# Optimization experiments

Measured on AMD Instinct MI355X. Metric: run time of the kernel, lower is better.

Reference implementation:

```python
import jax, jax.numpy as jnp
import numpy as np

B, S, H, E, V = 64, 1024, 1024, 1024, 50257


def setup_inputs() -> dict:
    key = jax.random.key(0)
    ks = jax.random.split(key, 12)
    x = jax.random.randint(ks[0], (B, 1), 0, V, dtype=jnp.int64)
    h = jax.random.normal(ks[1], (B, H), dtype=jnp.float32)
    c = jax.random.normal(ks[2], (B, H), dtype=jnp.float32)
    encoder_output = jax.random.normal(ks[3], (B, S, H), dtype=jnp.float32)
    length = jax.random.randint(ks[4], (B,), 1, S + 1, dtype=jnp.int32)
    length = length.at[0].set(S)  # mask width is length[0]; must equal S
    scale = 0.02
    emb = jax.random.normal(ks[5], (V, E), dtype=jnp.float32) * scale
    W_ih = jax.random.normal(ks[6], (4 * H, E), dtype=jnp.float32) * scale
    b_ih = jnp.zeros((4 * H,), dtype=jnp.float32)
    W_hh = jax.random.normal(ks[7], (4 * H, H), dtype=jnp.float32) * scale
    b_hh = jnp.zeros((4 * H,), dtype=jnp.float32)
    W_bilin = jax.random.normal(ks[8], (H, H), dtype=jnp.float32) * scale
    W_out = jax.random.normal(ks[9], (V, 2 * H), dtype=jnp.float32) * scale
    b_out = jnp.zeros((V,), dtype=jnp.float32)
    return {"x": x, "h": h, "c": c, "encoder_output": encoder_output,
            "length": length, "emb": emb, "W_ih": W_ih, "b_ih": b_ih,
            "W_hh": W_hh, "b_hh": b_hh, "W_bilin": W_bilin,
            "W_out": W_out, "b_out": b_out}


def reference(x, h, c, encoder_output, length, emb, W_ih, b_ih, W_hh, b_hh,
              W_bilin, W_out, b_out):
    # embedding + squeeze(1); dropout is identity in eval mode
    xe = emb[x[:, 0]]  # [B, E]
    # LSTMCell: gates in PyTorch order i, f, g, o
    gates = xe @ W_ih.T + b_ih + h @ W_hh.T + b_hh  # [B, 4H]
    i_g, f_g, g_g, o_g = jnp.split(gates, 4, axis=-1)
    i_g = jax.nn.sigmoid(i_g)
    f_g = jax.nn.sigmoid(f_g)
    g_g = jnp.tanh(g_g)
    o_g = jax.nn.sigmoid(o_g)
    c_new = f_g * c + i_g * g_g
    h_new = o_g * jnp.tanh(c_new)  # [B, H]
    # bilinear attention energy: (h W) . enc
    energy = jnp.einsum('bh,hk,bsk->bs', h_new, W_bilin, encoder_output)
    # mask multiplies energy BEFORE softmax (faithful to original code)
    mask = (jnp.arange(S)[None, :] < length[:, None]).astype(energy.dtype)
    attn = jax.nn.softmax(energy * mask, axis=-1)  # [B, S]
    context = jnp.einsum('bs,bsh->bh', attn, encoder_output)  # [B, H]
    output = jnp.concatenate([context, h_new], axis=1) @ W_out.T + b_out  # [B, V]
    return output, h_new, c_new
```

## Files before the change

### kernel.cpp

```cpp
#include <hip/hip_runtime.h>
#include <math.h>

constexpr int NB = 64;
constexpr int NS = 1024;
constexpr int NH = 1024;
constexpr int NE = 1024;
constexpr int NV = 50257;
constexpr int NK2 = 2048;

typedef __bf16 bf16_8 __attribute__((ext_vector_type(8)));
typedef float  f32x4  __attribute__((ext_vector_type(4)));

__global__ __launch_bounds__(256) void k_cvtAg(const int* __restrict__ x,
    const float* __restrict__ h, const float* __restrict__ emb,
    __bf16* __restrict__ Ag) {
  int t = blockIdx.x * 256 + threadIdx.x;
  int b = t >> 11, k = t & 2047;
  float v = (k < NE) ? emb[(size_t)x[b] * NE + k] : h[b * NH + (k - NE)];
  Ag[t] = (__bf16)v;
}

__global__ __launch_bounds__(256) void k_gates_mfma(const __bf16* __restrict__ Ag,
    const float* __restrict__ Wih, const float* __restrict__ bih,
    const float* __restrict__ Whh, const float* __restrict__ bhh,
    float* __restrict__ gates) {
  __shared__ f32x4 red[4][4][64];
  int lane = threadIdx.x & 63;
  int wave = threadIdx.x >> 6;
  int col  = lane & 15;
  int grp  = lane >> 4;
  int j    = blockIdx.x * 16 + col;

  const float* Wsel = (wave < 2) ? Wih : Whh;
  const float*  wp  = Wsel + (size_t)j * 1024 + (wave & 1) * 512 + grp * 8;
  const __bf16* ap  = Ag + wave * 512 + grp * 8;

  f32x4 acc[4] = {};
#pragma unroll 4
  for (int ks = 0; ks < 16; ++ks) {
    int kb = ks * 32;
    float4 b0 = *(const float4*)(wp + kb);
    float4 b1 = *(const float4*)(wp + kb + 4);
    bf16_8 bf;
    bf[0] = (__bf16)b0.x; bf[1] = (__bf16)b0.y;
    bf[2] = (__bf16)b0.z; bf[3] = (__bf16)b0.w;
    bf[4] = (__bf16)b1.x; bf[5] = (__bf16)b1.y;
    bf[6] = (__bf16)b1.z; bf[7] = (__bf16)b1.w;
#pragma unroll
    for (int m = 0; m < 4; ++m) {
      bf16_8 a = *(const bf16_8*)(ap + (m * 16 + col) * NK2 + kb);
      acc[m] = __builtin_amdgcn_mfma_f32_16x16x32_bf16(a, bf, acc[m], 0, 0, 0);
    }
  }
#pragma unroll
  for (int m = 0; m < 4; ++m) red[wave][m][lane] = acc[m];
  __syncthreads();
  f32x4 s = red[0][wave][lane];
#pragma unroll
  for (int wv = 1; wv < 4; ++wv) s += red[wv][wave][lane];
  float bias = bih[j] + bhh[j];
  int b = wave * 16 + grp * 4;
#pragma unroll
  for (int r = 0; r < 4; ++r)
    gates[(b + r) * 4096 + j] = s[r] + bias;
}

__global__ __launch_bounds__(256) void k_lstm(const float* __restrict__ gates,
    const float* __restrict__ c, float* __restrict__ hc_out,
    __bf16* __restrict__ A_bf) {
  int t = blockIdx.x * 256 + threadIdx.x;
  int b = t >> 10, hh = t & 1023;
  float ig = gates[b * 4096 + hh];
  float fg = gates[b * 4096 + 1024 + hh];
  float gg = gates[b * 4096 + 2048 + hh];
  float og = gates[b * 4096 + 3072 + hh];
  float i_ = 1.f / (1.f + expf(-ig));
  float f_ = 1.f / (1.f + expf(-fg));
  float g_ = tanhf(gg);
  float o_ = 1.f / (1.f + expf(-og));
  float cn = f_ * c[t] + i_ * g_;
  float hn = o_ * tanhf(cn);
  hc_out[t] = hn;
  hc_out[NB * NH + t] = cn;
  A_bf[b * NK2 + 1024 + hh] = (__bf16)hn;
}

__global__ __launch_bounds__(256) void k_bilin(const float* __restrict__ hnew,
    const float* __restrict__ Wb, float* __restrict__ t_out) {
  int b = blockIdx.x >> 2;
  int k = ((blockIdx.x & 3) << 8) + threadIdx.x;
  const float* hb = hnew + b * NH;
  float acc = 0.f;
#pragma unroll 8
  for (int hh = 0; hh < NH; ++hh)
    acc += hb[hh] * Wb[hh * NH + k];
  t_out[b * NH + k] = acc;
}

__global__ __launch_bounds__(256) void k_attn(const float* __restrict__ t_in,
    const float* __restrict__ enc, const int* __restrict__ length,
    float* __restrict__ ctxp, float* __restrict__ ml) {
  int b     = blockIdx.x >> 4;
  int strip = ((blockIdx.x & 15) << 2) + (threadIdx.x >> 6);
  int lane  = threadIdx.x & 63;
  int len   = length[b];
  int s0    = strip * 16;

  const float4* tp4 = (const float4*)(t_in + b * NH);
  float4 tv[4];
#pragma unroll
  for (int i = 0; i < 4; ++i) tv[i] = tp4[i * 64 + lane];

  const float4* ep4 = (const float4*)(enc + ((size_t)b * NS + s0) * NH);

  float m_run = -1e30f, l_run = 0.f;
  f32x4 acc[4] = {};

#pragma unroll 2
  for (int r = 0; r < 16; ++r) {
    float4 e[4];
#pragma unroll
    for (int i = 0; i < 4; ++i) e[i] = ep4[r * 256 + i * 64 + lane];
    float d = 0.f;
#pragma unroll
    for (int i = 0; i < 4; ++i)
      d += tv[i].x * e[i].x + tv[i].y * e[i].y + tv[i].z * e[i].z + tv[i].w * e[i].w;
#pragma unroll
    for (int off = 32; off; off >>= 1) d += __shfl_xor(d, off);
    float v = (s0 + r < len) ? d : 0.f;
    float m_new = fmaxf(m_run, v);
    float f = expf(m_run - m_new);
    float w = expf(v - m_new);
    l_run = l_run * f + w;
#pragma unroll
    for (int i = 0; i < 4; ++i) {
      acc[i][0] = acc[i][0] * f + w * e[i].x;
      acc[i][1] = acc[i][1] * f + w * e[i].y;
      acc[i][2] = acc[i][2] * f + w * e[i].z;
      acc[i][3] = acc[i][3] * f + w * e[i].w;
    }
    m_run = m_new;
  }

  int idx = b * 64 + strip;
  float* P = ctxp + (size_t)idx * 1024;
#pragma unroll
  for (int i = 0; i < 4; ++i)
    *(f32x4*)(P + (i * 64 + lane) * 4) = acc[i];
  if (lane == 0) {
    ml[idx * 2]     = m_run;
    ml[idx * 2 + 1] = l_run;
  }
}

__global__ __launch_bounds__(256) void k_attn_combine(const float* __restrict__ ctxp,
    const float* __restrict__ ml, __bf16* __restrict__ A_bf) {
  int b = blockIdx.x;
  int tid = threadIdx.x;
  float M = -1e30f;
#pragma unroll
  for (int c = 0; c < 64; ++c) M = fmaxf(M, ml[(b * 64 + c) * 2]);
  float Z = 0.f;
  f32x4 num = {0.f, 0.f, 0.f, 0.f};
#pragma unroll 4
  for (int c = 0; c < 64; ++c) {
    float e = expf(ml[(b * 64 + c) * 2] - M);
    Z += e * ml[(b * 64 + c) * 2 + 1];
    f32x4 p = *(const f32x4*)(ctxp + ((size_t)(b * 64 + c)) * 1024 + tid * 4);
    num += e * p;
  }
  float inv = 1.f / Z;
  __bf16* dst = A_bf + b * NK2 + tid * 4;
#pragma unroll
  for (int i = 0; i < 4; ++i) dst[i] = (__bf16)(num[i] * inv);
}

__global__ __launch_bounds__(64) void k_out_mfma(const __bf16* __restrict__ A,
    const float* __restrict__ Wout, const float* __restrict__ bout,
    float* __restrict__ out) {
  int lane = threadIdx.x;
  int col  = lane & 15;
  int grp  = lane >> 4;
  int vb   = blockIdx.x * 32;
  int va   = vb + col;
  int vc   = vb + 16 + col;
  int vaC  = va < NV ? va : NV - 1;
  int vcC  = vc < NV ? vc : NV - 1;

  const float*  wpA = Wout + (size_t)vaC * NK2 + grp * 8;
  const float*  wpB = Wout + (size_t)vcC * NK2 + grp * 8;
  const __bf16* ap  = A + grp * 8;

  f32x4 acc[4][2] = {};

#pragma unroll 2
  for (int ks = 0; ks < 64; ++ks) {
    int kb = ks * 32;
    float4 a0 = *(const float4*)(wpA + kb);
    float4 a1 = *(const float4*)(wpA + kb + 4);
    float4 c0 = *(const float4*)(wpB + kb);
    float4 c1 = *(const float4*)(wpB + kb + 4);
    bf16_8 bfA, bfB;
    bfA[0] = (__bf16)a0.x; bfA[1] = (__bf16)a0.y;
    bfA[2] = (__bf16)a0.z; bfA[3] = (__bf16)a0.w;
    bfA[4] = (__bf16)a1.x; bfA[5] = (__bf16)a1.y;
    bfA[6] = (__bf16)a1.z; bfA[7] = (__bf16)a1.w;
    bfB[0] = (__bf16)c0.x; bfB[1] = (__bf16)c0.y;
    bfB[2] = (__bf16)c0.z; bfB[3] = (__bf16)c0.w;
    bfB[4] = (__bf16)c1.x; bfB[5] = (__bf16)c1.y;
    bfB[6] = (__bf16)c1.z; bfB[7] = (__bf16)c1.w;
#pragma unroll
    for (int m = 0; m < 4; ++m) {
      bf16_8 a = *(const bf16_8*)(ap + (size_t)(m * 16 + col) * NK2 + kb);
      acc[m][0] = __builtin_amdgcn_mfma_f32_16x16x32_bf16(a, bfA, acc[m][0], 0, 0, 0);
      acc[m][1] = __builtin_amdgcn_mfma_f32_16x16x32_bf16(a, bfB, acc[m][1], 0, 0, 0);
    }
  }

#pragma unroll
  for (int n = 0; n < 2; ++n) {
    int vrow = vb + n * 16 + col;
    if (vrow < NV) {
      float bb = bout[vrow];
      int mrow = grp * 4;
#pragma unroll
      for (int m = 0; m < 4; ++m)
#pragma unroll
        for (int r = 0; r < 4; ++r)
          out[(size_t)(m * 16 + mrow + r) * NV + vrow] = acc[m][n][r] + bb;
    }
  }
}

extern "C" void kernel_launch(void* const* d_in, const int* in_sizes, int n_in,
                              void* d_out, int out_size, void* d_ws, size_t ws_size,
                              hipStream_t stream) {
  const int*   x      = (const int*)d_in[0];
  const float* h      = (const float*)d_in[1];
  const float* c      = (const float*)d_in[2];
  const float* enc    = (const float*)d_in[3];
  const int*   length = (const int*)d_in[4];
  const float* emb    = (const float*)d_in[5];
  const float* Wih    = (const float*)d_in[6];
  const float* bih    = (const float*)d_in[7];
  const float* Whh    = (const float*)d_in[8];
  const float* bhh    = (const float*)d_in[9];
  const float* Wb     = (const float*)d_in[10];
  const float* Wout   = (const float*)d_in[11];
  const float* bout   = (const float*)d_in[12];

  float* out = (float*)d_out;
  float* hn  = out + (size_t)NB * NV;

  float* ws      = (float*)d_ws;
  float* gates   = ws;
  float* t_ws    = gates + NB * 4 * NH;
  float* ctxp    = t_ws + NB * NH;
  float* ml      = ctxp + 64 * (size_t)NB * 1024;
  __bf16* A_bf   = (__bf16*)(ml + NB * 128);
  __bf16* Ag_bf  = A_bf + NB * NK2;

  k_cvtAg<<<NB * NK2 / 256, 256, 0, stream>>>(x, h, emb, Ag_bf);
  k_gates_mfma<<<4096 / 16, 256, 0, stream>>>(Ag_bf, Wih, bih, Whh, bhh, gates);
  k_lstm<<<NB * NH / 256, 256, 0, stream>>>(gates, c, hn, A_bf);
  k_bilin<<<NB * 4, 256, 0, stream>>>(hn, Wb, t_ws);
  k_attn<<<NB * 16, 256, 0, stream>>>(t_ws, enc, length, ctxp, ml);
  k_attn_combine<<<NB, 256, 0, stream>>>(ctxp, ml, A_bf);
  k_out_mfma<<<(NV + 31) / 32, 64, 0, stream>>>(A_bf, Wout, bout, out);
}
```

Baseline: 308.1 us.

## Split attention into finer strips and restructure output GEMM with prefetch

Measured after the change: 351.2 us. 1.14x slower.

```diff
diff --git a/kernel.cpp b/kernel.cpp
--- a/kernel.cpp
+++ b/kernel.cpp
@@ -100,11 +100,11 @@
 __global__ __launch_bounds__(256) void k_attn(const float* __restrict__ t_in,
     const float* __restrict__ enc, const int* __restrict__ length,
     float* __restrict__ ctxp, float* __restrict__ ml) {
-  int b     = blockIdx.x >> 4;
-  int strip = ((blockIdx.x & 15) << 2) + (threadIdx.x >> 6);
+  int b     = blockIdx.x >> 5;
+  int strip = ((blockIdx.x & 31) << 2) + (threadIdx.x >> 6);
   int lane  = threadIdx.x & 63;
   int len   = length[b];
-  int s0    = strip * 16;
+  int s0    = strip * 8;
 
   const float4* tp4 = (const float4*)(t_in + b * NH);
   float4 tv[4];
@@ -117,7 +117,7 @@
   f32x4 acc[4] = {};
 
 #pragma unroll 2
-  for (int r = 0; r < 16; ++r) {
+  for (int r = 0; r < 8; ++r) {
     float4 e[4];
 #pragma unroll
     for (int i = 0; i < 4; ++i) e[i] = ep4[r * 256 + i * 64 + lane];
@@ -142,7 +142,7 @@
     m_run = m_new;
   }
 
-  int idx = b * 64 + strip;
+  int idx = b * 128 + strip;
   float* P = ctxp + (size_t)idx * 1024;
 #pragma unroll
   for (int i = 0; i < 4; ++i)
@@ -158,15 +158,15 @@
   int b = blockIdx.x;
   int tid = threadIdx.x;
   float M = -1e30f;
-#pragma unroll
-  for (int c = 0; c < 64; ++c) M = fmaxf(M, ml[(b * 64 + c) * 2]);
+#pragma unroll 8
+  for (int c = 0; c < 128; ++c) M = fmaxf(M, ml[(b * 128 + c) * 2]);
   float Z = 0.f;
   f32x4 num = {0.f, 0.f, 0.f, 0.f};
 #pragma unroll 4
-  for (int c = 0; c < 64; ++c) {
-    float e = expf(ml[(b * 64 + c) * 2] - M);
-    Z += e * ml[(b * 64 + c) * 2 + 1];
-    f32x4 p = *(const f32x4*)(ctxp + ((size_t)(b * 64 + c)) * 1024 + tid * 4);
+  for (int c = 0; c < 128; ++c) {
+    float e = expf(ml[(b * 128 + c) * 2] - M);
+    Z += e * ml[(b * 128 + c) * 2 + 1];
+    f32x4 p = *(const f32x4*)(ctxp + ((size_t)(b * 128 + c)) * 1024 + tid * 4);
     num += e * p;
   }
   float inv = 1.f / Z;
@@ -175,60 +175,70 @@
   for (int i = 0; i < 4; ++i) dst[i] = (__bf16)(num[i] * inv);
 }
 
-__global__ __launch_bounds__(64) void k_out_mfma(const __bf16* __restrict__ A,
+__global__ __launch_bounds__(256) void k_out_mfma(const __bf16* __restrict__ A,
     const float* __restrict__ Wout, const float* __restrict__ bout,
     float* __restrict__ out) {
-  int lane = threadIdx.x;
+  int lane = threadIdx.x & 63;
+  int wave = threadIdx.x >> 6;
   int col  = lane & 15;
   int grp  = lane >> 4;
-  int vb   = blockIdx.x * 32;
-  int va   = vb + col;
-  int vc   = vb + 16 + col;
-  int vaC  = va < NV ? va : NV - 1;
-  int vcC  = vc < NV ? vc : NV - 1;
-
-  const float*  wpA = Wout + (size_t)vaC * NK2 + grp * 8;
-  const float*  wpB = Wout + (size_t)vcC * NK2 + grp * 8;
-  const __bf16* ap  = A + grp * 8;
-
-  f32x4 acc[4][2] = {};
+  int vrow = blockIdx.x * 64 + wave * 16 + col;
+  int vcl  = vrow < NV ? vrow : NV - 1;
+
+  const float*  wp = Wout + (size_t)vcl * NK2 + grp * 8;
+  const __bf16* ap = A + grp * 8;
+
+  f32x4 acc[4] = {};
+
+  float4 w0 = *(const float4*)(wp);
+  float4 w1 = *(const float4*)(wp + 4);
+  bf16_8 a[4];
+#pragma unroll
+  for (int m = 0; m < 4; ++m)
+    a[m] = *(const bf16_8*)(ap + (size_t)(m * 16 + col) * NK2);
 
 #pragma unroll 2
-  for (int ks = 0; ks < 64; ++ks) {
-    int kb = ks * 32;
-    float4 a0 = *(const float4*)(wpA + kb);
-    float4 a1 = *(const float4*)(wpA + kb + 4);
-    float4 c0 = *(const float4*)(wpB + kb);
-    float4 c1 = *(const float4*)(wpB + kb + 4);
-    bf16_8 bfA, bfB;
-    bfA[0] = (__bf16)a0.x; bfA[1] = (__bf16)a0.y;
-    bfA[2] = (__bf16)a0.z; bfA[3] = (__bf16)a0.w;
-    bfA[4] = (__bf16)a1.x; bfA[5] = (__bf16)a1.y;
-    bfA[6] = (__bf16)a1.z; bfA[7] = (__bf16)a1.w;
-    bfB[0] = (__bf16)c0.x; bfB[1] = (__bf16)c0.y;
-    bfB[2] = (__bf16)c0.z; bfB[3] = (__bf16)c0.w;
-    bfB[4] = (__bf16)c1.x; bfB[5] = (__bf16)c1.y;
-    bfB[6] = (__bf16)c1.z; bfB[7] = (__bf16)c1.w;
-#pragma unroll
-    for (int m = 0; m < 4; ++m) {
-      bf16_8 a = *(const bf16_8*)(ap + (size_t)(m * 16 + col) * NK2 + kb);
-      acc[m][0] = __builtin_amdgcn_mfma_f32_16x16x32_bf16(a, bfA, acc[m][0], 0, 0, 0);
-      acc[m][1] = __builtin_amdgcn_mfma_f32_16x16x32_bf16(a, bfB, acc[m][1], 0, 0, 0);
-    }
-  }
-
-#pragma unroll
-  for (int n = 0; n < 2; ++n) {
-    int vrow = vb + n * 16 + col;
-    if (vrow < NV) {
-      float bb = bout[vrow];
-      int mrow = grp * 4;
-#pragma unroll
-      for (int m = 0; m < 4; ++m)
-#pragma unroll
-        for (int r = 0; r < 4; ++r)
-          out[(size_t)(m * 16 + mrow + r) * NV + vrow] = acc[m][n][r] + bb;
-    }
+  for (int ks = 0; ks < 63; ++ks) {
+    int kb = (ks + 1) * 32;
+    float4 nw0 = *(const float4*)(wp + kb);
+    float4 nw1 = *(const float4*)(wp + kb + 4);
+    bf16_8 na[4];
+#pragma unroll
+    for (int m = 0; m < 4; ++m)
+      na[m] = *(const bf16_8*)(ap + (size_t)(m * 16 + col) * NK2 + kb);
+
+    bf16_8 bf;
+    bf[0] = (__bf16)w0.x; bf[1] = (__bf16)w0.y;
+    bf[2] = (__bf16)w0.z; bf[3] = (__bf16)w0.w;
+    bf[4] = (__bf16)w1.x; bf[5] = (__bf16)w1.y;
+    bf[6] = (__bf16)w1.z; bf[7] = (__bf16)w1.w;
+#pragma unroll
+    for (int m = 0; m < 4; ++m)
+      acc[m] = __builtin_amdgcn_mfma_f32_16x16x32_bf16(a[m], bf, acc[m], 0, 0, 0);
+
+    w0 = nw0; w1 = nw1;
+#pragma unroll
+    for (int m = 0; m < 4; ++m) a[m] = na[m];
+  }
+  {
+    bf16_8 bf;
+    bf[0] = (__bf16)w0.x; bf[1] = (__bf16)w0.y;
+    bf[2] = (__bf16)w0.z; bf[3] = (__bf16)w0.w;
+    bf[4] = (__bf16)w1.x; bf[5] = (__bf16)w1.y;
+    bf[6] = (__bf16)w1.z; bf[7] = (__bf16)w1.w;
+#pragma unroll
+    for (int m = 0; m < 4; ++m)
+      acc[m] = __builtin_amdgcn_mfma_f32_16x16x32_bf16(a[m], bf, acc[m], 0, 0, 0);
+  }
+
+  if (vrow < NV) {
+    float bb = bout[vrow];
+    int mrow = grp * 4;
+#pragma unroll
+    for (int m = 0; m < 4; ++m)
+#pragma unroll
+      for (int r = 0; r < 4; ++r)
+        out[(size_t)(m * 16 + mrow + r) * NV + vrow] = acc[m][r] + bb;
   }
 }
 
@@ -256,15 +266,15 @@
   float* gates   = ws;
   float* t_ws    = gates + NB * 4 * NH;
   float* ctxp    = t_ws + NB * NH;
-  float* ml      = ctxp + 64 * (size_t)NB * 1024;
-  __bf16* A_bf   = (__bf16*)(ml + NB * 128);
+  float* ml      = ctxp + 128 * (size_t)NB * 1024;
+  __bf16* A_bf   = (__bf16*)(ml + NB * 256);
   __bf16* Ag_bf  = A_bf + NB * NK2;
 
   k_cvtAg<<<NB * NK2 / 256, 256, 0, stream>>>(x, h, emb, Ag_bf);
   k_gates_mfma<<<4096 / 16, 256, 0, stream>>>(Ag_bf, Wih, bih, Whh, bhh, gates);
   k_lstm<<<NB * NH / 256, 256, 0, stream>>>(gates, c, hn, A_bf);
   k_bilin<<<NB * 4, 256, 0, stream>>>(hn, Wb, t_ws);
-  k_attn<<<NB * 16, 256, 0, stream>>>(t_ws, enc, length, ctxp, ml);
+  k_attn<<<NB * 32, 256, 0, stream>>>(t_ws, enc, length, ctxp, ml);
   k_attn_combine<<<NB, 256, 0, stream>>>(ctxp, ml, A_bf);
-  k_out_mfma<<<(NV + 31) / 32, 64, 0, stream>>>(A_bf, Wout, bout, out);
-}
+  k_out_mfma<<<(NV + 63) / 64, 256, 0, stream>>>(A_bf, Wout, bout, out);
+}
```
